# Optimization experiments

Measured on AMD Instinct MI355X. Metric: run time of the kernel, lower is better.

The kernel has to match this reference:

```python
import jax, jax.numpy as jnp
import numpy as np

B0 = 2048
B1 = 2048


def _param(k, shape, fan_in):
    return jax.random.normal(k, shape, dtype=jnp.float32) / np.float32(np.sqrt(fan_in))


def setup_inputs() -> dict:
    key = jax.random.key(0)
    ks = jax.random.split(key, 32)
    inp = {
        'zw_0': jax.random.normal(ks[0], (B0, 128), dtype=jnp.float32),
        'zw_1': jax.random.normal(ks[1], (B1, 128), dtype=jnp.float32),
        'c': jax.random.normal(ks[2], (B0 + B1, 64), dtype=jnp.float32),
        # Wk: Linear(64 -> 128)
        'Wk_w': _param(ks[3], (128, 64), 64), 'Wk_b': jnp.zeros((128,), jnp.float32),
        # Ww[0], Ww[1]: Linear(64 -> 128)
        'Ww0_w': _param(ks[4], (128, 64), 64), 'Ww0_b': jnp.zeros((128,), jnp.float32),
        'Ww1_w': _param(ks[5], (128, 64), 64), 'Ww1_b': jnp.zeros((128,), jnp.float32),
        # linear_0/1: Linear(128 -> 64) + ReLU
        'lin0_w': _param(ks[6], (64, 128), 128), 'lin0_b': jnp.zeros((64,), jnp.float32),
        'lin1_w': _param(ks[7], (64, 128), 128), 'lin1_b': jnp.zeros((64,), jnp.float32),
        # attention_0/1: Linear(64->32), Tanh, Linear(32->1)
        'a0_1w': _param(ks[8], (32, 64), 64), 'a0_1b': jnp.zeros((32,), jnp.float32),
        'a0_2w': _param(ks[9], (1, 32), 32), 'a0_2b': jnp.zeros((1,), jnp.float32),
        'a1_1w': _param(ks[10], (32, 64), 64), 'a1_1b': jnp.zeros((32,), jnp.float32),
        'a1_2w': _param(ks[11], (1, 32), 32), 'a1_2b': jnp.zeros((1,), jnp.float32),
    }
    return inp


def _loo_pool(zw, lw, lb, a1w, a1b, a2w, a2b):
    # zt = ReLU(Linear(128->64))  [B, 64]
    zt = jax.nn.relu(zw @ lw.T + lb)
    # attention score per row  [B]
    s = (jnp.tanh(zt @ a1w.T + a1b) @ a2w.T + a2b)[:, 0]
    B = zt.shape[0]
    # leave-one-out softmax: row i attends over all j != i (diag masked to -inf)
    logits = jnp.where(jnp.eye(B, dtype=bool), -jnp.inf, jnp.broadcast_to(s[None, :], (B, B)))
    w = jax.nn.softmax(logits, axis=1)  # [B, B]
    return w @ zt  # [B, 64]


def reference(zw_0, zw_1, c,
              Wk_w, Wk_b, Ww0_w, Ww0_b, Ww1_w, Ww1_b,
              lin0_w, lin0_b, lin1_w, lin1_b,
              a0_1w, a0_1b, a0_2w, a0_2b,
              a1_1w, a1_1b, a1_2w, a1_2b):
    b0 = zw_0.shape[0]
    pooled0 = _loo_pool(zw_0, lin0_w, lin0_b, a0_1w, a0_1b, a0_2w, a0_2b)
    pooled1 = _loo_pool(zw_1, lin1_w, lin1_b, a1_1w, a1_1b, a1_2w, a1_2b)
    ck = c @ Wk_w.T + Wk_b  # [B, 128]
    pred0 = pooled0 @ Ww0_w.T + Ww0_b + ck[:b0]
    pred1 = pooled1 @ Ww1_w.T + Ww1_b + ck[b0:]
    pred = jnp.concatenate([pred0, pred1], axis=0)  # [B, 128]
    zw = jnp.concatenate([zw_0, zw_1], axis=0)      # [B, 128]
    total = zw @ pred.T                              # [B, B]
    batch = total.shape[0]
    nce_w = -jnp.sum(jnp.diagonal(jax.nn.log_softmax(total, axis=1))) / batch
    return nce_w
```

## Files before the change

kernel.cpp:

```cpp
#include <hip/hip_runtime.h>
#include <math.h>

#define B_TOT 4096
#define B_HALF 2048

#define ZWB_OFF    0
#define EV_OFF     262144
#define VV_OFF     266240
#define BASE_OFF   790528
#define PSTAT_OFF  1314816
#define PREDB_OFF  1347840
#define DIAG_OFF   1609984
#define ACC_OFF    1614080
#define TICKET_OFF 1614081

typedef __bf16 bf16x8 __attribute__((ext_vector_type(8)));
typedef float  f32x4  __attribute__((ext_vector_type(4)));

__device__ __forceinline__ unsigned short f2bf(float f) {
    unsigned u = __float_as_uint(f);
    u = u + 0x7fffu + ((u >> 16) & 1u);
    return (unsigned short)(u >> 16);
}
__device__ __forceinline__ float bf2f(unsigned short h) {
    return __uint_as_float(((unsigned)h) << 16);
}

__global__ __launch_bounds__(256)
void k1(const float* __restrict__ zw0, const float* __restrict__ zw1,
        const float* __restrict__ c,
        const float* __restrict__ Wk_w, const float* __restrict__ Wk_b,
        const float* __restrict__ Ww0_w, const float* __restrict__ Ww0_b,
        const float* __restrict__ Ww1_w, const float* __restrict__ Ww1_b,
        const float* __restrict__ lin0_w, const float* __restrict__ lin0_b,
        const float* __restrict__ lin1_w, const float* __restrict__ lin1_b,
        const float* __restrict__ a0_1w, const float* __restrict__ a0_1b,
        const float* __restrict__ a0_2w, const float* __restrict__ a0_2b,
        const float* __restrict__ a1_1w, const float* __restrict__ a1_1b,
        const float* __restrict__ a1_2w, const float* __restrict__ a1_2b,
        float* __restrict__ ws) {
    __shared__ float lws[8448];
    __shared__ float zws[2112];
    __shared__ float ztl[1088];
    __shared__ float a1s[2176];
    __shared__ float wbuf[8704];
    __shared__ float cl[1088];
    __shared__ float el[16];
    __shared__ float part[256];
    int tid = threadIdx.x;
    int b = blockIdx.x;
    int base = b * 16;
    int g = (base >= B_HALF);
    const float* lw = g ? lin1_w : lin0_w;
    const float* lb = g ? lin1_b : lin0_b;
    const float* w1 = g ? a1_1w : a0_1w;
    const float* b1 = g ? a1_1b : a0_1b;
    const float* w2 = g ? a1_2w : a0_2w;
    const float* b2 = g ? a1_2b : a0_2b;
    const float* Ww  = g ? Ww1_w : Ww0_w;
    const float* Wwb = g ? Ww1_b : Ww0_b;
    unsigned short* zwb = (unsigned short*)(ws + ZWB_OFF);

    const float4* lw4 = (const float4*)lw;
    for (int i = tid; i < 2048; i += 256) {
        int o = i >> 5, k4 = i & 31;
        ((float4*)(lws + o * 132))[k4] = lw4[i];
    }
    for (int i = tid; i < 512; i += 256) {
        int r = i >> 5, k4 = i & 31;
        int gi = base + r;
        const float* zr = (gi < B_HALF) ? (zw0 + (size_t)gi * 128)
                                        : (zw1 + (size_t)(gi - B_HALF) * 128);
        float4 v = ((const float4*)zr)[k4];
        ((float4*)(zws + r * 132))[k4] = v;
        uint2 p;
        p.x = (unsigned)f2bf(v.x) | ((unsigned)f2bf(v.y) << 16);
        p.y = (unsigned)f2bf(v.z) | ((unsigned)f2bf(v.w) << 16);
        ((uint2*)(zwb + (size_t)gi * 128))[k4] = p;
    }
    const float4* w14 = (const float4*)w1;
    for (int i = tid; i < 512; i += 256) {
        int o = i >> 4, k4 = i & 15;
        ((float4*)(a1s + o * 68))[k4] = w14[i];
    }
    if (tid < 256) {
        int r = tid >> 4, k4 = tid & 15;
        ((float4*)(cl + r * 68))[k4] = ((const float4*)(c + (size_t)(base + r) * 64))[k4];
    }
    const float4* Wk4 = (const float4*)Wk_w;
    for (int i = tid; i < 2048; i += 256) {
        int o = i >> 4, k4 = i & 15;
        ((float4*)(wbuf + o * 68))[k4] = Wk4[i];
    }
    __syncthreads();

    {
        int o = tid & 63, rgrp = tid >> 6;
        float bias = lb[o];
        float acc[4] = {bias, bias, bias, bias};
        const float4* wrow = (const float4*)(lws + o * 132);
        const float4* zr0 = (const float4*)(zws + (rgrp + 0) * 132);
        const float4* zr1 = (const float4*)(zws + (rgrp + 4) * 132);
        const float4* zr2 = (const float4*)(zws + (rgrp + 8) * 132);
        const float4* zr3 = (const float4*)(zws + (rgrp + 12) * 132);
#pragma unroll 4
        for (int k4 = 0; k4 < 32; ++k4) {
            float4 wv = wrow[k4];
            float4 z0 = zr0[k4], z1 = zr1[k4], z2 = zr2[k4], z3 = zr3[k4];
            acc[0] = fmaf(wv.x, z0.x, fmaf(wv.y, z0.y, fmaf(wv.z, z0.z, fmaf(wv.w, z0.w, acc[0]))));
            acc[1] = fmaf(wv.x, z1.x, fmaf(wv.y, z1.y, fmaf(wv.z, z1.z, fmaf(wv.w, z1.w, acc[1]))));
            acc[2] = fmaf(wv.x, z2.x, fmaf(wv.y, z2.y, fmaf(wv.z, z2.z, fmaf(wv.w, z2.w, acc[2]))));
            acc[3] = fmaf(wv.x, z3.x, fmaf(wv.y, z3.y, fmaf(wv.z, z3.z, fmaf(wv.w, z3.w, acc[3]))));
        }
#pragma unroll
        for (int rr = 0; rr < 4; ++rr)
            ztl[(rgrp + rr * 4) * 68 + o] = fmaxf(acc[rr], 0.f);
    }
    __syncthreads();

    {
        int o2 = tid & 31, r2 = tid >> 5;
        const float4* arow = (const float4*)(a1s + o2 * 68);
#pragma unroll
        for (int rpass = 0; rpass < 2; ++rpass) {
            int row = r2 + rpass * 8;
            float a = b1[o2];
            const float4* zt4 = (const float4*)(ztl + row * 68);
#pragma unroll 4
            for (int k4 = 0; k4 < 16; ++k4) {
                float4 wv = arow[k4];
                float4 zv = zt4[k4];
                a = fmaf(wv.x, zv.x, fmaf(wv.y, zv.y, fmaf(wv.z, zv.z, fmaf(wv.w, zv.w, a))));
            }
            float h = tanhf(a) * w2[o2];
#pragma unroll
            for (int mask = 16; mask > 0; mask >>= 1) h += __shfl_xor(h, mask);
            if (o2 == 0) {
                float e = __expf(h + b2[0]);
                el[row] = e;
                ws[EV_OFF + base + row] = e;
            }
        }
    }

    {
        int o = tid & 127, rsel = tid >> 7;
        float bias = Wk_b[o] + Wwb[o];
        float acc[8] = {bias, bias, bias, bias, bias, bias, bias, bias};
        const float4* krow = (const float4*)(wbuf + o * 68);
#pragma unroll 4
        for (int k4 = 0; k4 < 16; ++k4) {
            float4 kv = krow[k4];
#pragma unroll
            for (int j = 0; j < 8; ++j) {
                float4 cv = ((const float4*)(cl + (rsel + j * 2) * 68))[k4];
                acc[j] = fmaf(kv.x, cv.x, fmaf(kv.y, cv.y, fmaf(kv.z, cv.z, fmaf(kv.w, cv.w, acc[j]))));
            }
        }
#pragma unroll
        for (int j = 0; j < 8; ++j)
            ws[BASE_OFF + (size_t)(base + rsel + j * 2) * 128 + o] = acc[j];
    }
    __syncthreads();

    const float4* Ww4 = (const float4*)Ww;
    for (int i = tid; i < 2048; i += 256) {
        int o = i >> 4, k4 = i & 15;
        ((float4*)(wbuf + o * 68))[k4] = Ww4[i];
    }
    __syncthreads();

    {
        int o = tid & 127, rsel = tid >> 7;
        float acc[8] = {0.f, 0.f, 0.f, 0.f, 0.f, 0.f, 0.f, 0.f};
        const float4* wrow = (const float4*)(wbuf + o * 68);
#pragma unroll 4
        for (int k4 = 0; k4 < 16; ++k4) {
            float4 wv = wrow[k4];
#pragma unroll
            for (int j = 0; j < 8; ++j) {
                float4 pv = ((const float4*)(ztl + (rsel + j * 2) * 68))[k4];
                acc[j] = fmaf(wv.x, pv.x, fmaf(wv.y, pv.y, fmaf(wv.z, pv.z, fmaf(wv.w, pv.w, acc[j]))));
            }
        }
        float p = 0.f;
#pragma unroll
        for (int j = 0; j < 8; ++j) {
            ws[VV_OFF + (size_t)(base + rsel + j * 2) * 128 + o] = acc[j];
            p = fmaf(el[rsel + j * 2], acc[j], p);
        }
        part[tid] = p;
    }
    __syncthreads();
    if (tid < 128)
        ws[PSTAT_OFF + (size_t)b * 129 + 1 + tid] = part[tid] + part[tid + 128];
    if (tid == 128) {
        float E = 0.f;
#pragma unroll
        for (int r = 0; r < 16; ++r) E += el[r];
        ws[PSTAT_OFF + (size_t)b * 129] = E;
    }
}

__global__ __launch_bounds__(256)
void k2(float* __restrict__ ws) {
    __shared__ float us[132];
    int tid = threadIdx.x;
    int b = blockIdx.x;
    int base = b * 16;
    int g = (b >= 128);
    unsigned short* zwb   = (unsigned short*)(ws + ZWB_OFF);
    unsigned short* predb = (unsigned short*)(ws + PREDB_OFF);

    if (tid < 129) {
        const float* ps = ws + PSTAT_OFF + (size_t)g * 128 * 129 + tid;
        float acc = 0.f;
#pragma unroll 8
        for (int q = 0; q < 128; ++q) acc += ps[(size_t)q * 129];
        us[tid] = acc;
    }
    if (b == 0 && tid == 200) {
        ws[ACC_OFF] = 0.f;
        ws[TICKET_OFF] = 0.f;
    }
    __syncthreads();

    float E = us[0];
    int r = tid >> 4, s16 = tid & 15;
    int gi = base + r;
    float er = ws[EV_OFF + gi];
    float inv = 1.f / (E - er);
    int o8 = s16 * 8;
    const float4* v4 = (const float4*)(ws + VV_OFF + (size_t)gi * 128 + o8);
    const float4* b4 = (const float4*)(ws + BASE_OFF + (size_t)gi * 128 + o8);
    float pr[8];
#pragma unroll
    for (int h = 0; h < 2; ++h) {
        float4 vv = v4[h], bb = b4[h];
        pr[h * 4 + 0] = (us[1 + o8 + h * 4 + 0] - er * vv.x) * inv + bb.x;
        pr[h * 4 + 1] = (us[1 + o8 + h * 4 + 1] - er * vv.y) * inv + bb.y;
        pr[h * 4 + 2] = (us[1 + o8 + h * 4 + 2] - er * vv.z) * inv + bb.z;
        pr[h * 4 + 3] = (us[1 + o8 + h * 4 + 3] - er * vv.w) * inv + bb.w;
    }
    uint4 pk;
    pk.x = (unsigned)f2bf(pr[0]) | ((unsigned)f2bf(pr[1]) << 16);
    pk.y = (unsigned)f2bf(pr[2]) | ((unsigned)f2bf(pr[3]) << 16);
    pk.z = (unsigned)f2bf(pr[4]) | ((unsigned)f2bf(pr[5]) << 16);
    pk.w = (unsigned)f2bf(pr[6]) | ((unsigned)f2bf(pr[7]) << 16);
    ((uint4*)(predb + (size_t)gi * 128))[s16] = pk;

    uint4 zz = ((const uint4*)(zwb + (size_t)gi * 128))[s16];
    const unsigned* zu = (const unsigned*)&zz;
    float d = 0.f;
#pragma unroll
    for (int q = 0; q < 4; ++q) {
        d = fmaf(bf2f((unsigned short)(zu[q] & 0xffff)), pr[q * 2], d);
        d = fmaf(bf2f((unsigned short)(zu[q] >> 16)), pr[q * 2 + 1], d);
    }
#pragma unroll
    for (int mask = 8; mask > 0; mask >>= 1) d += __shfl_xor(d, mask);
    if (s16 == 0) ws[DIAG_OFF + gi] = d;
}

__global__ __launch_bounds__(1024, 1)
void k3(float* __restrict__ ws, float* __restrict__ out) {
    __shared__ unsigned short zs[8704];
    __shared__ unsigned short ps[4][8704];
    __shared__ float2 part2[256];
    int tid = threadIdx.x;
    int i0 = blockIdx.x * 64;
    const unsigned short* zwb   = (const unsigned short*)(ws + ZWB_OFF);
    const unsigned short* predb = (const unsigned short*)(ws + PREDB_OFF);

    {
        int r = tid >> 4, q = tid & 15;
        ((float4*)(zs + r * 136))[q] = ((const float4*)(zwb + (size_t)(i0 + r) * 128))[q];
    }

    int w = tid >> 6, lane = tid & 63;
    int g = w >> 2, wl = w & 3;
    int m16 = lane & 15, quad = lane >> 4;
    int tg = tid & 255;
    int prow = tg >> 2, pq4 = (tg & 3) * 4;
    unsigned short* psg = ps[g];

    float4 pf[4];
    {
        const float4* src = (const float4*)(predb + (size_t)(g * 1024 + prow) * 128);
#pragma unroll
        for (int k = 0; k < 4; ++k) pf[k] = src[pq4 + k];
#pragma unroll
        for (int k = 0; k < 4; ++k) ((float4*)(psg + prow * 136))[pq4 + k] = pf[k];
    }
    __syncthreads();

    bf16x8 af[4];
#pragma unroll
    for (int kk = 0; kk < 4; ++kk)
        af[kk] = *((const bf16x8*)(zs + (wl * 16 + m16) * 136 + kk * 32 + quad * 8));

    float m_run[4], s_run[4];
#pragma unroll
    for (int r = 0; r < 4; ++r) { m_run[r] = -INFINITY; s_run[r] = 0.f; }

    for (int jt = 0; jt < 16; ++jt) {
        if (jt < 15) {
            const float4* src =
                (const float4*)(predb + (size_t)(g * 1024 + (jt + 1) * 64 + prow) * 128);
#pragma unroll
            for (int k = 0; k < 4; ++k) pf[k] = src[pq4 + k];
        }
        f32x4 acc[4];
#pragma unroll
        for (int b4 = 0; b4 < 4; ++b4) {
            acc[b4] = (f32x4){0.f, 0.f, 0.f, 0.f};
#pragma unroll
            for (int kk = 0; kk < 4; ++kk) {
                bf16x8 bf = *((const bf16x8*)(psg + (b4 * 16 + m16) * 136 + kk * 32 + quad * 8));
                acc[b4] = __builtin_amdgcn_mfma_f32_16x16x32_bf16(af[kk], bf, acc[b4], 0, 0, 0);
            }
        }
#pragma unroll
        for (int r = 0; r < 4; ++r) {
            float vm = fmaxf(fmaxf(acc[0][r], acc[1][r]), fmaxf(acc[2][r], acc[3][r]));
            float mn = fmaxf(m_run[r], vm);
            float add = __expf(acc[0][r] - mn) + __expf(acc[1][r] - mn) +
                        __expf(acc[2][r] - mn) + __expf(acc[3][r] - mn);
            s_run[r] = s_run[r] * __expf(m_run[r] - mn) + add;
            m_run[r] = mn;
        }
        __syncthreads();
        if (jt < 15) {
#pragma unroll
            for (int k = 0; k < 4; ++k) ((float4*)(psg + prow * 136))[pq4 + k] = pf[k];
        }
        __syncthreads();
    }

#pragma unroll
    for (int r = 0; r < 4; ++r) {
        float m = m_run[r], s = s_run[r];
#pragma unroll
        for (int mask = 1; mask < 16; mask <<= 1) {
            float om = __shfl_xor(m, mask);
            float os = __shfl_xor(s, mask);
            float mn = fmaxf(m, om);
            s = s * __expf(m - mn) + os * __expf(om - mn);
            m = mn;
        }
        if (m16 == 0) {
            int row = wl * 16 + quad * 4 + r;
            part2[row * 4 + g] = make_float2(m, s);
        }
    }
    __syncthreads();

    if (tid < 64) {
        float M = -INFINITY;
#pragma unroll
        for (int q = 0; q < 4; ++q) M = fmaxf(M, part2[tid * 4 + q].x);
        float S = 0.f;
#pragma unroll
        for (int q = 0; q < 4; ++q)
            S += part2[tid * 4 + q].y * __expf(part2[tid * 4 + q].x - M);
        float rowval = ws[DIAG_OFF + i0 + tid] - (M + logf(S));
#pragma unroll
        for (int mask = 32; mask > 0; mask >>= 1)
            rowval += __shfl_xor(rowval, mask);
        if (tid == 0) {
            atomicAdd(ws + ACC_OFF, rowval);
            __threadfence();
            unsigned old = atomicAdd((unsigned*)(ws + TICKET_OFF), 1u);
            if (old == 63u) {
                __threadfence();
                float acc = __hip_atomic_load(ws + ACC_OFF, __ATOMIC_RELAXED,
                                              __HIP_MEMORY_SCOPE_AGENT);
                out[0] = -acc / (float)B_TOT;
            }
        }
    }
}

extern "C" void kernel_launch(void* const* d_in, const int* in_sizes, int n_in,
                              void* d_out, int out_size, void* d_ws, size_t ws_size,
                              hipStream_t stream) {
    const float* zw_0   = (const float*)d_in[0];
    const float* zw_1   = (const float*)d_in[1];
    const float* c      = (const float*)d_in[2];
    const float* Wk_w   = (const float*)d_in[3];
    const float* Wk_b   = (const float*)d_in[4];
    const float* Ww0_w  = (const float*)d_in[5];
    const float* Ww0_b  = (const float*)d_in[6];
    const float* Ww1_w  = (const float*)d_in[7];
    const float* Ww1_b  = (const float*)d_in[8];
    const float* lin0_w = (const float*)d_in[9];
    const float* lin0_b = (const float*)d_in[10];
    const float* lin1_w = (const float*)d_in[11];
    const float* lin1_b = (const float*)d_in[12];
    const float* a0_1w  = (const float*)d_in[13];
    const float* a0_1b  = (const float*)d_in[14];
    const float* a0_2w  = (const float*)d_in[15];
    const float* a0_2b  = (const float*)d_in[16];
    const float* a1_1w  = (const float*)d_in[17];
    const float* a1_1b  = (const float*)d_in[18];
    const float* a1_2w  = (const float*)d_in[19];
    const float* a1_2b  = (const float*)d_in[20];
    float* ws  = (float*)d_ws;
    float* out = (float*)d_out;

    k1<<<256, 256, 0, stream>>>(zw_0, zw_1, c, Wk_w, Wk_b,
                                Ww0_w, Ww0_b, Ww1_w, Ww1_b,
                                lin0_w, lin0_b, lin1_w, lin1_b,
                                a0_1w, a0_1b, a0_2w, a0_2b,
                                a1_1w, a1_1b, a1_2w, a1_2b, ws);
    k2<<<256, 256, 0, stream>>>(ws);
    k3<<<64, 1024, 0, stream>>>(ws, out);
}
```

Before: 175.0 us.

## Split NCE logsumexp across 2D grid with register-resident tiles and final reduce kernel

```diff
diff --git a/kernel.cpp b/kernel.cpp
--- a/kernel.cpp
+++ b/kernel.cpp
@@ -11,8 +11,7 @@
 #define PSTAT_OFF  1314816
 #define PREDB_OFF  1347840
 #define DIAG_OFF   1609984
-#define ACC_OFF    1614080
-#define TICKET_OFF 1614081
+#define PART_OFF   1614080
 
 typedef __bf16 bf16x8 __attribute__((ext_vector_type(8)));
 typedef float  f32x4  __attribute__((ext_vector_type(4)));
@@ -219,10 +218,6 @@
         for (int q = 0; q < 128; ++q) acc += ps[(size_t)q * 129];
         us[tid] = acc;
     }
-    if (b == 0 && tid == 200) {
-        ws[ACC_OFF] = 0.f;
-        ws[TICKET_OFF] = 0.f;
-    }
     __syncthreads();
 
     float E = us[0];
@@ -262,100 +257,92 @@
     if (s16 == 0) ws[DIAG_OFF + gi] = d;
 }
 
-__global__ __launch_bounds__(1024, 1)
-void k3(float* __restrict__ ws, float* __restrict__ out) {
-    __shared__ unsigned short zs[8704];
-    __shared__ unsigned short ps[4][8704];
-    __shared__ float2 part2[256];
+__global__ __launch_bounds__(512, 2)
+void k3(float* __restrict__ ws) {
+    __shared__ float2 part2[128 * 4];
     int tid = threadIdx.x;
-    int i0 = blockIdx.x * 64;
+    int b = blockIdx.x;
+    int ic = b >> 3, jc = b & 7;
+    int i0 = ic * 128;
+    int w = tid >> 6, lane = tid & 63;
+    int rowg = w >> 2, jsub = w & 3;
+    int rowbase = i0 + rowg * 64;
+    int jbase = jc * 512 + jsub * 128;
+    int m16 = lane & 15, quad = lane >> 4;
     const unsigned short* zwb   = (const unsigned short*)(ws + ZWB_OFF);
     const unsigned short* predb = (const unsigned short*)(ws + PREDB_OFF);
 
-    {
-        int r = tid >> 4, q = tid & 15;
-        ((float4*)(zs + r * 136))[q] = ((const float4*)(zwb + (size_t)(i0 + r) * 128))[q];
-    }
-
-    int w = tid >> 6, lane = tid & 63;
-    int g = w >> 2, wl = w & 3;
-    int m16 = lane & 15, quad = lane >> 4;
-    int tg = tid & 255;
-    int prow = tg >> 2, pq4 = (tg & 3) * 4;
-    unsigned short* psg = ps[g];
-
-    float4 pf[4];
-    {
-        const float4* src = (const float4*)(predb + (size_t)(g * 1024 + prow) * 128);
-#pragma unroll
-        for (int k = 0; k < 4; ++k) pf[k] = src[pq4 + k];
-#pragma unroll
-        for (int k = 0; k < 4; ++k) ((float4*)(psg + prow * 136))[pq4 + k] = pf[k];
-    }
-    __syncthreads();
-
-    bf16x8 af[4];
+    bf16x8 af[4][4];
+#pragma unroll
+    for (int a = 0; a < 4; ++a)
+#pragma unroll
+        for (int kk = 0; kk < 4; ++kk)
+            af[a][kk] = *((const bf16x8*)(zwb +
+                (size_t)(rowbase + a * 16 + m16) * 128 + kk * 32 + quad * 8));
+
+    float m_run[4][4], s_run[4][4];
+#pragma unroll
+    for (int a = 0; a < 4; ++a)
+#pragma unroll
+        for (int r = 0; r < 4; ++r) { m_run[a][r] = -INFINITY; s_run[a][r] = 0.f; }
+
+    bf16x8 pf[4];
 #pragma unroll
     for (int kk = 0; kk < 4; ++kk)
-        af[kk] = *((const bf16x8*)(zs + (wl * 16 + m16) * 136 + kk * 32 + quad * 8));
-
-    float m_run[4], s_run[4];
-#pragma unroll
-    for (int r = 0; r < 4; ++r) { m_run[r] = -INFINITY; s_run[r] = 0.f; }
-
-    for (int jt = 0; jt < 16; ++jt) {
-        if (jt < 15) {
-            const float4* src =
-                (const float4*)(predb + (size_t)(g * 1024 + (jt + 1) * 64 + prow) * 128);
-#pragma unroll
-            for (int k = 0; k < 4; ++k) pf[k] = src[pq4 + k];
+        pf[kk] = *((const bf16x8*)(predb +
+            (size_t)(jbase + m16) * 128 + kk * 32 + quad * 8));
+
+    for (int jt = 0; jt < 8; ++jt) {
+        bf16x8 bf[4];
+#pragma unroll
+        for (int kk = 0; kk < 4; ++kk) bf[kk] = pf[kk];
+        if (jt < 7) {
+            int jrow = jbase + (jt + 1) * 16 + m16;
+#pragma unroll
+            for (int kk = 0; kk < 4; ++kk)
+                pf[kk] = *((const bf16x8*)(predb +
+                    (size_t)jrow * 128 + kk * 32 + quad * 8));
         }
         f32x4 acc[4];
 #pragma unroll
-        for (int b4 = 0; b4 < 4; ++b4) {
-            acc[b4] = (f32x4){0.f, 0.f, 0.f, 0.f};
-#pragma unroll
-            for (int kk = 0; kk < 4; ++kk) {
-                bf16x8 bf = *((const bf16x8*)(psg + (b4 * 16 + m16) * 136 + kk * 32 + quad * 8));
-                acc[b4] = __builtin_amdgcn_mfma_f32_16x16x32_bf16(af[kk], bf, acc[b4], 0, 0, 0);
-            }
-        }
+        for (int a = 0; a < 4; ++a) acc[a] = (f32x4){0.f, 0.f, 0.f, 0.f};
+#pragma unroll
+        for (int kk = 0; kk < 4; ++kk)
+#pragma unroll
+            for (int a = 0; a < 4; ++a)
+                acc[a] = __builtin_amdgcn_mfma_f32_16x16x32_bf16(af[a][kk], bf[kk], acc[a], 0, 0, 0);
+#pragma unroll
+        for (int a = 0; a < 4; ++a)
+#pragma unroll
+            for (int r = 0; r < 4; ++r) {
+                float v = acc[a][r];
+                float mn = fmaxf(m_run[a][r], v);
+                s_run[a][r] = s_run[a][r] * __expf(m_run[a][r] - mn) + __expf(v - mn);
+                m_run[a][r] = mn;
+            }
+    }
+
+#pragma unroll
+    for (int a = 0; a < 4; ++a)
 #pragma unroll
         for (int r = 0; r < 4; ++r) {
-            float vm = fmaxf(fmaxf(acc[0][r], acc[1][r]), fmaxf(acc[2][r], acc[3][r]));
-            float mn = fmaxf(m_run[r], vm);
-            float add = __expf(acc[0][r] - mn) + __expf(acc[1][r] - mn) +
-                        __expf(acc[2][r] - mn) + __expf(acc[3][r] - mn);
-            s_run[r] = s_run[r] * __expf(m_run[r] - mn) + add;
-            m_run[r] = mn;
-        }
-        __syncthreads();
-        if (jt < 15) {
-#pragma unroll
-            for (int k = 0; k < 4; ++k) ((float4*)(psg + prow * 136))[pq4 + k] = pf[k];
-        }
-        __syncthreads();
-    }
-
-#pragma unroll
-    for (int r = 0; r < 4; ++r) {
-        float m = m_run[r], s = s_run[r];
-#pragma unroll
-        for (int mask = 1; mask < 16; mask <<= 1) {
-            float om = __shfl_xor(m, mask);
-            float os = __shfl_xor(s, mask);
-            float mn = fmaxf(m, om);
-            s = s * __expf(m - mn) + os * __expf(om - mn);
-            m = mn;
-        }
-        if (m16 == 0) {
-            int row = wl * 16 + quad * 4 + r;
-            part2[row * 4 + g] = make_float2(m, s);
-        }
-    }
-    __syncthreads();
-
-    if (tid < 64) {
+            float m = m_run[a][r], s = s_run[a][r];
+#pragma unroll
+            for (int mask = 1; mask < 16; mask <<= 1) {
+                float om = __shfl_xor(m, mask);
+                float os = __shfl_xor(s, mask);
+                float mn = fmaxf(m, om);
+                s = s * __expf(m - mn) + os * __expf(om - mn);
+                m = mn;
+            }
+            if (m16 == 0) {
+                int rib = rowg * 64 + a * 16 + quad * 4 + r;
+                part2[rib * 4 + jsub] = make_float2(m, s);
+            }
+        }
+    __syncthreads();
+
+    if (tid < 128) {
         float M = -INFINITY;
 #pragma unroll
         for (int q = 0; q < 4; ++q) M = fmaxf(M, part2[tid * 4 + q].x);
@@ -363,22 +350,32 @@
 #pragma unroll
         for (int q = 0; q < 4; ++q)
             S += part2[tid * 4 + q].y * __expf(part2[tid * 4 + q].x - M);
-        float rowval = ws[DIAG_OFF + i0 + tid] - (M + logf(S));
-#pragma unroll
-        for (int mask = 32; mask > 0; mask >>= 1)
-            rowval += __shfl_xor(rowval, mask);
-        if (tid == 0) {
-            atomicAdd(ws + ACC_OFF, rowval);
-            __threadfence();
-            unsigned old = atomicAdd((unsigned*)(ws + TICKET_OFF), 1u);
-            if (old == 63u) {
-                __threadfence();
-                float acc = __hip_atomic_load(ws + ACC_OFF, __ATOMIC_RELAXED,
-                                              __HIP_MEMORY_SCOPE_AGENT);
-                out[0] = -acc / (float)B_TOT;
-            }
-        }
-    }
+        ((float2*)(ws + PART_OFF))[(size_t)(i0 + tid) * 8 + jc] = make_float2(M, S);
+    }
+}
+
+__global__ __launch_bounds__(1024)
+void k4(const float* __restrict__ ws, float* __restrict__ out) {
+    __shared__ float red[1024];
+    int tid = threadIdx.x;
+    float acc = 0.f;
+    for (int r = tid; r < B_TOT; r += 1024) {
+        const float2* p = (const float2*)(ws + PART_OFF) + (size_t)r * 8;
+        float M = -INFINITY;
+#pragma unroll
+        for (int q = 0; q < 8; ++q) M = fmaxf(M, p[q].x);
+        float S = 0.f;
+#pragma unroll
+        for (int q = 0; q < 8; ++q) S += p[q].y * __expf(p[q].x - M);
+        acc += ws[DIAG_OFF + r] - (M + logf(S));
+    }
+    red[tid] = acc;
+    __syncthreads();
+    for (int o = 512; o > 0; o >>= 1) {
+        if (tid < o) red[tid] += red[tid + o];
+        __syncthreads();
+    }
+    if (tid == 0) out[0] = -red[0] / (float)B_TOT;
 }
 
 extern "C" void kernel_launch(void* const* d_in, const int* in_sizes, int n_in,
@@ -414,5 +411,6 @@
                                 a0_1w, a0_1b, a0_2w, a0_2b,
                                 a1_1w, a1_1b, a1_2w, a1_2b, ws);
     k2<<<256, 256, 0, stream>>>(ws);
-    k3<<<64, 1024, 0, stream>>>(ws, out);
-}
+    k3<<<256, 512, 0, stream>>>(ws);
+    k4<<<1, 1024, 0, stream>>>(ws, out);
+}
```

After: 141.4 us, median of 2. 1.24x faster.
